# Kernel optimization log

Measured on AMD Instinct MI355X. Metric: run time of the kernel, lower is better.

Reference implementation:

```python
import jax, jax.numpy as jnp
import numpy as np

DIM = 512
HEADS = 8
DIM_HEAD = 64
INNER = HEADS * DIM_HEAD  # 512


def setup_inputs() -> dict:
    key = jax.random.key(0)
    k1, k2, k3 = jax.random.split(key, 3)
    B, N = 4, 2048
    x = jax.random.normal(k1, (B, N, DIM), dtype=jnp.float32)
    # nn.Linear(dim, inner*3, bias=False): weight shape [3*inner, dim]; y = x @ W.T
    w_qkv = jax.random.normal(k2, (3 * INNER, DIM), dtype=jnp.float32) * (DIM ** -0.5)
    # to_out: nn.Linear(inner, dim) with bias
    w_out = jax.random.normal(k3, (DIM, INNER), dtype=jnp.float32) * (INNER ** -0.5)
    b_out = jnp.zeros((DIM,), dtype=jnp.float32)
    return {"x": x, "w_qkv": w_qkv, "w_out": w_out, "b_out": b_out}


def reference(x, w_qkv, w_out, b_out):
    B, N, C = x.shape
    scale = DIM_HEAD ** -0.5
    qkv = jnp.einsum('bnc,fc->bnf', x, w_qkv)  # [B, N, 3*inner]
    qkv = qkv.reshape(B, N, 3, HEADS, DIM_HEAD).transpose(2, 0, 3, 1, 4)  # [3,B,H,N,D]
    q, k, v = qkv[0], qkv[1], qkv[2]
    dots = jnp.einsum('bhnd,bhmd->bhnm', q, k) * scale  # [B,H,N,N]
    attn = jax.nn.softmax(dots, axis=-1)
    out = jnp.einsum('bhnm,bhmd->bhnd', attn, v)  # [B,H,N,D]
    out = out.transpose(0, 2, 1, 3).reshape(B, N, C)
    return jnp.einsum('bnf,cf->bnc', out, w_out) + b_out
```

## Files before the change

kernel.cpp:

```cpp
#include <hip/hip_runtime.h>


typedef __bf16 bf16x8 __attribute__((ext_vector_type(8)));
typedef __bf16 bf16x4v __attribute__((ext_vector_type(4)));
typedef float f32x4 __attribute__((ext_vector_type(4)));
typedef unsigned int u32;
typedef unsigned short u16;
typedef u32 u32x2v __attribute__((ext_vector_type(2)));
typedef u32 u32x4v __attribute__((ext_vector_type(4)));

__device__ __forceinline__ u16 f2bf(float f) {
  union { float f; u32 u; } v; v.f = f;
  u32 r = v.u + 0x7FFFu + ((v.u >> 16) & 1u);
  return (u16)(r >> 16);
}

__device__ __forceinline__ u32x2v pack4bf(float a, float b, float c, float d) {
  bf16x4v v; v[0] = (__bf16)a; v[1] = (__bf16)b; v[2] = (__bf16)c; v[3] = (__bf16)d;
  return __builtin_bit_cast(u32x2v, v);
}

__device__ __forceinline__ f32x4 mfma16(bf16x8 a, bf16x8 b, f32x4 c) {
  return __builtin_amdgcn_mfma_f32_16x16x32_bf16(a, b, c, 0, 0, 0);
}

__device__ __forceinline__ void swap32(u32& a, u32& b) {
  u32x2v r = __builtin_amdgcn_permlane32_swap(a, b, false, false);
  a = r[0]; b = r[1];
}
__device__ __forceinline__ void swap16(u32& a, u32& b) {
  u32x2v r = __builtin_amdgcn_permlane16_swap(a, b, false, false);
  a = r[0]; b = r[1];
}

__global__ void convert_all(const float4* __restrict__ x, const float4* __restrict__ wq,
                            const float4* __restrict__ wo, u16* __restrict__ xb,
                            u16* __restrict__ wqb, u16* __restrict__ wob) {
  int t = blockIdx.x * blockDim.x + threadIdx.x;
  float4 v; u16* dst;
  if (t < 1048576)        { v = x[t];             dst = xb  + (size_t)t * 4; }
  else if (t < 1245184)   { int u = t - 1048576; v = wq[u]; dst = wqb + (size_t)u * 4; }
  else                    { int u = t - 1245184; v = wo[u]; dst = wob + (size_t)u * 4; }
  u32x2v o2;
  o2[0] = (u32)f2bf(v.x) | ((u32)f2bf(v.y) << 16);
  o2[1] = (u32)f2bf(v.z) | ((u32)f2bf(v.w) << 16);
  *(u32x2v*)dst = o2;
}

template<int MODE>
__global__ __launch_bounds__(256, 2) void gemm_nt(
    const u16* __restrict__ A, const u16* __restrict__ B,
    float* __restrict__ Cf, u16* __restrict__ Cb, u16* __restrict__ Vt,
    const float* __restrict__ bias, int M, int N, int K)
{
  __shared__ __align__(16) u16 As[128 * 64];
  __shared__ __align__(16) u16 Bs[128 * 64];
  const int tid = threadIdx.x;
  const int w = tid >> 6, lane = tid & 63, g = lane >> 4, c = lane & 15;
  const int wr = w >> 1, wc = w & 1;
  const int byy = blockIdx.y;
  const int by = (byy & 7) * 8 + (byy >> 3);
  const long m0 = (long)by * 128;
  const long n0 = (long)blockIdx.x * 128;
  const f32x4 zero4 = {0.f, 0.f, 0.f, 0.f};

  f32x4 acc[4][4];
#pragma unroll
  for (int i = 0; i < 4; ++i)
#pragma unroll
    for (int j = 0; j < 4; ++j) acc[i][j] = zero4;

  const int srow = tid >> 3;
  const int sch  = (tid & 7) * 8;

#pragma unroll 1
  for (int kk = 0; kk < K; kk += 64) {
#pragma unroll
    for (int i = 0; i < 4; ++i) {
      __builtin_amdgcn_global_load_lds(
          (__attribute__((address_space(1))) void*)(A + (m0 + i * 32 + srow) * K + kk + sch),
          (__attribute__((address_space(3))) void*)(As + (i * 32 + w * 8) * 64),
          16, 0, 0);
      __builtin_amdgcn_global_load_lds(
          (__attribute__((address_space(1))) void*)(B + (n0 + i * 32 + srow) * K + kk + sch),
          (__attribute__((address_space(3))) void*)(Bs + (i * 32 + w * 8) * 64),
          16, 0, 0);
    }
    __syncthreads();

#pragma unroll
    for (int ks = 0; ks < 2; ++ks) {
      bf16x8 af[4], bfr[4];
#pragma unroll
      for (int mi = 0; mi < 4; ++mi)
        af[mi] = *(const bf16x8*)&As[(wr * 64 + mi * 16 + c) * 64 + ks * 32 + g * 8];
#pragma unroll
      for (int nj = 0; nj < 4; ++nj)
        bfr[nj] = *(const bf16x8*)&Bs[(wc * 64 + nj * 16 + c) * 64 + ks * 32 + g * 8];
#pragma unroll
      for (int mi = 0; mi < 4; ++mi)
#pragma unroll
        for (int nj = 0; nj < 4; ++nj)
          acc[mi][nj] = mfma16(af[mi], bfr[nj], acc[mi][nj]);
    }
    __syncthreads();
  }

#pragma unroll
  for (int mi = 0; mi < 4; ++mi)
#pragma unroll
    for (int nj = 0; nj < 4; ++nj) {
      const long rowb = m0 + wr * 64 + mi * 16 + g * 4;
      const long col  = n0 + wc * 64 + nj * 16 + c;
      if (MODE == 1) {
#pragma unroll
        for (int r = 0; r < 4; ++r)
          Cf[(rowb + r) * N + col] = acc[mi][nj][r] + bias[col];
      } else if (n0 < 512) {
#pragma unroll
        for (int r = 0; r < 4; ++r)
          Cb[(rowb + r) * N + col] = f2bf(acc[mi][nj][r] * 0.18033688f);
      } else if (n0 < 1024) {
#pragma unroll
        for (int r = 0; r < 4; ++r)
          Cb[(rowb + r) * N + col] = f2bf(acc[mi][nj][r]);
      } else {
        u32x2v pk;
        pk[0] = (u32)f2bf(acc[mi][nj][0]) | ((u32)f2bf(acc[mi][nj][1]) << 16);
        pk[1] = (u32)f2bf(acc[mi][nj][2]) | ((u32)f2bf(acc[mi][nj][3]) << 16);
        *(u32x2v*)&Vt[(col - 1024) * 8192 + rowb] = pk;
      }
    }
}

__global__ __launch_bounds__(256, 2) void attn_fwd(const u16* __restrict__ qkv,
                                                   const u16* __restrict__ Vt,
                                                   u16* __restrict__ ao)
{
  __shared__ __align__(16) u16 SH[32768 / 2];
  char* const shb = (char*)SH;

  const int tid = threadIdx.x;
  const int w = tid >> 6, lane = tid & 63, g = lane >> 4, c = lane & 15;

  const int swz = (blockIdx.x & 7) * 64 + (blockIdx.x >> 3);
  const int bh = swz >> 4;
  const int qb = swz & 15;
  const long rowbase = (long)(bh >> 3) * 2048;
  const int hcol = (bh & 7) * 64;
  const int q0 = qb * 128 + w * 32;
  const f32x4 zero4 = {0.f, 0.f, 0.f, 0.f};

  bf16x8 qf[2][2];
#pragma unroll
  for (int sub = 0; sub < 2; ++sub)
#pragma unroll
    for (int ks = 0; ks < 2; ++ks)
      qf[sub][ks] = *(const bf16x8*)(qkv + (rowbase + q0 + sub * 16 + c) * 1536 + hcol + ks * 32 + g * 8);

  float lsum[2] = {0.f, 0.f};
  f32x4 o[2][4];
#pragma unroll
  for (int sub = 0; sub < 2; ++sub)
#pragma unroll
    for (int n = 0; n < 4; ++n) o[sub][n] = zero4;

  const u16* kbase = qkv + rowbase * 1536 + 512 + hcol;
  const u16* vtb   = Vt + (long)hcol * 8192 + rowbase;

  const int srow8 = lane >> 3;
  const int schk8 = ((lane & 7) ^ srow8) * 8;
  const int swzc = (c & 7) << 4;

  const int rd0 = c * 128 + ((g * 16) ^ swzc);
  const int rd1 = c * 128 + ((64 + g * 16) ^ swzc);

  const long r0 = w * 16 + srow8;
  const long r1 = w * 16 + 8 + srow8;
  const u16* kp0 = kbase + (64 + r0) * 1536 + schk8;
  const u16* kp1 = kbase + (64 + r1) * 1536 + schk8;
  const u16* vg0 = vtb + r0 * 8192 + 64 + schk8;
  const u16* vg1 = vtb + r1 * 8192 + 64 + schk8;

  __builtin_amdgcn_global_load_lds(
      (__attribute__((address_space(1))) void*)(kbase + r0 * 1536 + schk8),
      (__attribute__((address_space(3))) void*)(shb + (w * 2 + 0) * 1024), 16, 0, 0);
  __builtin_amdgcn_global_load_lds(
      (__attribute__((address_space(1))) void*)(kbase + r1 * 1536 + schk8),
      (__attribute__((address_space(3))) void*)(shb + (w * 2 + 1) * 1024), 16, 0, 0);
  __builtin_amdgcn_global_load_lds(
      (__attribute__((address_space(1))) void*)(vtb + r0 * 8192 + schk8),
      (__attribute__((address_space(3))) void*)(shb + 16384 + (w * 2 + 0) * 1024), 16, 0, 0);
  __builtin_amdgcn_global_load_lds(
      (__attribute__((address_space(1))) void*)(vtb + r1 * 8192 + schk8),
      (__attribute__((address_space(3))) void*)(shb + 16384 + (w * 2 + 1) * 1024), 16, 0, 0);
  __syncthreads();

  bf16x8 vp[4][2];
  bf16x8 pa[2][2];

#pragma unroll 2
  for (int t = 0; t < 32; ++t) {
    const int buf = t & 1;
    const int KB = buf * 8192;
    const int VB = 16384 + buf * 8192;
    const int KN = 8192 - KB;
    const int VN = 16384 + (8192 - (VB - 16384));

    if (t < 31) {
      __builtin_amdgcn_global_load_lds(
          (__attribute__((address_space(1))) void*)kp0,
          (__attribute__((address_space(3))) void*)(shb + KN + (w * 2 + 0) * 1024), 16, 0, 0);
      __builtin_amdgcn_global_load_lds(
          (__attribute__((address_space(1))) void*)kp1,
          (__attribute__((address_space(3))) void*)(shb + KN + (w * 2 + 1) * 1024), 16, 0, 0);
      __builtin_amdgcn_global_load_lds(
          (__attribute__((address_space(1))) void*)vg0,
          (__attribute__((address_space(3))) void*)(shb + VN + (w * 2 + 0) * 1024), 16, 0, 0);
      __builtin_amdgcn_global_load_lds(
          (__attribute__((address_space(1))) void*)vg1,
          (__attribute__((address_space(3))) void*)(shb + VN + (w * 2 + 1) * 1024), 16, 0, 0);
      kp0 += 64 * 1536; kp1 += 64 * 1536;
      vg0 += 64;        vg1 += 64;
    }

    if (t > 0) {
      __builtin_amdgcn_s_setprio(1);
#pragma unroll
      for (int sub = 0; sub < 2; ++sub)
#pragma unroll
        for (int ks = 0; ks < 2; ++ks)
#pragma unroll
          for (int n = 0; n < 4; ++n)
            o[sub][n] = mfma16(vp[n][ks], pa[sub][ks], o[sub][n]);
      __builtin_amdgcn_s_setprio(0);
    }

    bf16x8 bk[4][2];
#pragma unroll
    for (int n = 0; n < 4; ++n) {
      bk[n][0] = *(const bf16x8*)(shb + KB + n * 2048 + rd0);
      bk[n][1] = *(const bf16x8*)(shb + KB + n * 2048 + rd1);
    }

    f32x4 s[2][4];
    __builtin_amdgcn_s_setprio(1);
#pragma unroll
    for (int sub = 0; sub < 2; ++sub)
#pragma unroll
      for (int n = 0; n < 4; ++n) {
        f32x4 a0 = zero4;
        a0 = mfma16(bk[n][0], qf[sub][0], a0);
        a0 = mfma16(bk[n][1], qf[sub][1], a0);
        s[sub][n] = a0;
      }
    __builtin_amdgcn_s_setprio(0);

#pragma unroll
    for (int sub = 0; sub < 2; ++sub) {
      float rs = 0.f;
      u32 L[4], H[4];
#pragma unroll
      for (int n = 0; n < 4; ++n) {
        float p0 = __builtin_amdgcn_exp2f(s[sub][n][0]);
        float p1 = __builtin_amdgcn_exp2f(s[sub][n][1]);
        float p2 = __builtin_amdgcn_exp2f(s[sub][n][2]);
        float p3 = __builtin_amdgcn_exp2f(s[sub][n][3]);
        rs += (p0 + p1) + (p2 + p3);
        u32x2v pk = pack4bf(p0, p1, p2, p3);
        L[n] = pk[0]; H[n] = pk[1];
      }
      lsum[sub] += rs;
      swap32(L[0], L[1]); swap16(L[0], L[1]);
      swap32(H[0], H[1]); swap16(H[0], H[1]);
      swap32(L[2], L[3]); swap16(L[2], L[3]);
      swap32(H[2], H[3]); swap16(H[2], H[3]);
      u32x4v f0 = {L[0], H[0], L[1], H[1]};
      u32x4v f1 = {L[2], H[2], L[3], H[3]};
      pa[sub][0] = __builtin_bit_cast(bf16x8, f0);
      pa[sub][1] = __builtin_bit_cast(bf16x8, f1);
    }

#pragma unroll
    for (int n = 0; n < 4; ++n) {
      vp[n][0] = *(const bf16x8*)(shb + VB + n * 2048 + rd0);
      vp[n][1] = *(const bf16x8*)(shb + VB + n * 2048 + rd1);
    }

    __syncthreads();
  }

  __builtin_amdgcn_s_setprio(1);
#pragma unroll
  for (int sub = 0; sub < 2; ++sub)
#pragma unroll
    for (int ks = 0; ks < 2; ++ks)
#pragma unroll
      for (int n = 0; n < 4; ++n)
        o[sub][n] = mfma16(vp[n][ks], pa[sub][ks], o[sub][n]);
  __builtin_amdgcn_s_setprio(0);

#pragma unroll
  for (int sub = 0; sub < 2; ++sub) {
    float ls = lsum[sub];
    ls += __shfl_xor(ls, 16);
    ls += __shfl_xor(ls, 32);
    const float linv = 1.0f / ls;
    u16* aor = ao + (rowbase + q0 + sub * 16 + c) * 512 + hcol;
#pragma unroll
    for (int n = 0; n < 4; ++n) {
      u32x2v pk = pack4bf(o[sub][n][0] * linv, o[sub][n][1] * linv,
                          o[sub][n][2] * linv, o[sub][n][3] * linv);
      *(u32x2v*)&aor[n * 16 + g * 4] = pk;
    }
  }
}

extern "C" void kernel_launch(void* const* d_in, const int* in_sizes, int n_in,
                              void* d_out, int out_size, void* d_ws, size_t ws_size,
                              hipStream_t stream) {
  (void)in_sizes; (void)n_in; (void)out_size; (void)ws_size;
  const float* x    = (const float*)d_in[0];
  const float* wqkv = (const float*)d_in[1];
  const float* wout = (const float*)d_in[2];
  const float* bout = (const float*)d_in[3];

  char* ws = (char*)d_ws;
  u16* Xb  = (u16*)(ws);
  u16* Wqb = (u16*)(ws + (8ull << 20));
  u16* Wob = (u16*)(ws + (9ull << 20) + (512ull << 10));
  u16* QKV = (u16*)(ws + (10ull << 20));
  u16* Vt  = (u16*)(ws + (34ull << 20));
  u16* AO  = (u16*)(ws);

  convert_all<<<5120, 256, 0, stream>>>((const float4*)x, (const float4*)wqkv,
                                        (const float4*)wout, Xb, Wqb, Wob);
  gemm_nt<0><<<dim3(12, 64), 256, 0, stream>>>(Xb, Wqb, nullptr, QKV, Vt, nullptr, 8192, 1536, 512);
  attn_fwd<<<512, 256, 0, stream>>>(QKV, Vt, AO);
  gemm_nt<1><<<dim3(4, 64), 256, 0, stream>>>(AO, Wob, (float*)d_out, nullptr, nullptr, bout, 8192, 512, 512);
}
```

Measured before the change: 89.83 us.

## Split KV range across two wave groups per block and merge partials in LDS

The attention block grows from 4 to 8 waves. The two groups of four waves each stream half of the key/value sequence into their own double-buffered LDS region, so the loop runs 16 iterations instead of 32. At the end, the second group writes its partial output accumulators and row sums to LDS, and the first group adds them before normalising and storing. Because the softmax does not subtract a running max, the partials can simply be summed. This doubles the waves per CU to hide latency, at the cost of twice the LDS per block, a tighter register budget from the new launch bounds, and an extra reduction step.

```diff
diff --git a/kernel.cpp b/kernel.cpp
--- a/kernel.cpp
+++ b/kernel.cpp
@@ -133,22 +133,26 @@
     }
 }
 
-__global__ __launch_bounds__(256, 2) void attn_fwd(const u16* __restrict__ qkv,
+__global__ __launch_bounds__(512, 4) void attn_fwd(const u16* __restrict__ qkv,
                                                    const u16* __restrict__ Vt,
                                                    u16* __restrict__ ao)
 {
-  __shared__ __align__(16) u16 SH[32768 / 2];
+  __shared__ __align__(16) u16 SH[65536 / 2];
   char* const shb = (char*)SH;
 
   const int tid = threadIdx.x;
   const int w = tid >> 6, lane = tid & 63, g = lane >> 4, c = lane & 15;
+  const int g2 = w >> 2;
+  const int wq = w & 3;
+  const int GB = g2 << 15;
 
   const int swz = (blockIdx.x & 7) * 64 + (blockIdx.x >> 3);
   const int bh = swz >> 4;
   const int qb = swz & 15;
   const long rowbase = (long)(bh >> 3) * 2048;
   const int hcol = (bh & 7) * 64;
-  const int q0 = qb * 128 + w * 32;
+  const int q0 = qb * 128 + wq * 32;
+  const long kvb = (long)g2 * 1024;
   const f32x4 zero4 = {0.f, 0.f, 0.f, 0.f};
 
   bf16x8 qf[2][2];
@@ -172,54 +176,54 @@
   const int schk8 = ((lane & 7) ^ srow8) * 8;
   const int swzc = (c & 7) << 4;
 
-  const int rd0 = c * 128 + ((g * 16) ^ swzc);
-  const int rd1 = c * 128 + ((64 + g * 16) ^ swzc);
-
-  const long r0 = w * 16 + srow8;
-  const long r1 = w * 16 + 8 + srow8;
-  const u16* kp0 = kbase + (64 + r0) * 1536 + schk8;
-  const u16* kp1 = kbase + (64 + r1) * 1536 + schk8;
-  const u16* vg0 = vtb + r0 * 8192 + 64 + schk8;
-  const u16* vg1 = vtb + r1 * 8192 + 64 + schk8;
+  const int rdG0 = GB + c * 128 + ((g * 16) ^ swzc);
+  const int rdG1 = GB + c * 128 + ((64 + g * 16) ^ swzc);
+
+  const long r0 = wq * 16 + srow8;
+  const long r1 = wq * 16 + 8 + srow8;
+  const u16* kp0 = kbase + (kvb + 64 + r0) * 1536 + schk8;
+  const u16* kp1 = kbase + (kvb + 64 + r1) * 1536 + schk8;
+  const u16* vg0 = vtb + r0 * 8192 + kvb + 64 + schk8;
+  const u16* vg1 = vtb + r1 * 8192 + kvb + 64 + schk8;
 
   __builtin_amdgcn_global_load_lds(
-      (__attribute__((address_space(1))) void*)(kbase + r0 * 1536 + schk8),
-      (__attribute__((address_space(3))) void*)(shb + (w * 2 + 0) * 1024), 16, 0, 0);
+      (__attribute__((address_space(1))) void*)(kbase + (kvb + r0) * 1536 + schk8),
+      (__attribute__((address_space(3))) void*)(shb + GB + (wq * 2 + 0) * 1024), 16, 0, 0);
   __builtin_amdgcn_global_load_lds(
-      (__attribute__((address_space(1))) void*)(kbase + r1 * 1536 + schk8),
-      (__attribute__((address_space(3))) void*)(shb + (w * 2 + 1) * 1024), 16, 0, 0);
+      (__attribute__((address_space(1))) void*)(kbase + (kvb + r1) * 1536 + schk8),
+      (__attribute__((address_space(3))) void*)(shb + GB + (wq * 2 + 1) * 1024), 16, 0, 0);
   __builtin_amdgcn_global_load_lds(
-      (__attribute__((address_space(1))) void*)(vtb + r0 * 8192 + schk8),
-      (__attribute__((address_space(3))) void*)(shb + 16384 + (w * 2 + 0) * 1024), 16, 0, 0);
+      (__attribute__((address_space(1))) void*)(vtb + r0 * 8192 + kvb + schk8),
+      (__attribute__((address_space(3))) void*)(shb + GB + 16384 + (wq * 2 + 0) * 1024), 16, 0, 0);
   __builtin_amdgcn_global_load_lds(
-      (__attribute__((address_space(1))) void*)(vtb + r1 * 8192 + schk8),
-      (__attribute__((address_space(3))) void*)(shb + 16384 + (w * 2 + 1) * 1024), 16, 0, 0);
+      (__attribute__((address_space(1))) void*)(vtb + r1 * 8192 + kvb + schk8),
+      (__attribute__((address_space(3))) void*)(shb + GB + 16384 + (wq * 2 + 1) * 1024), 16, 0, 0);
   __syncthreads();
 
   bf16x8 vp[4][2];
   bf16x8 pa[2][2];
 
 #pragma unroll 2
-  for (int t = 0; t < 32; ++t) {
+  for (int t = 0; t < 16; ++t) {
     const int buf = t & 1;
     const int KB = buf * 8192;
     const int VB = 16384 + buf * 8192;
     const int KN = 8192 - KB;
     const int VN = 16384 + (8192 - (VB - 16384));
 
-    if (t < 31) {
+    if (t < 15) {
       __builtin_amdgcn_global_load_lds(
           (__attribute__((address_space(1))) void*)kp0,
-          (__attribute__((address_space(3))) void*)(shb + KN + (w * 2 + 0) * 1024), 16, 0, 0);
+          (__attribute__((address_space(3))) void*)(shb + GB + KN + (wq * 2 + 0) * 1024), 16, 0, 0);
       __builtin_amdgcn_global_load_lds(
           (__attribute__((address_space(1))) void*)kp1,
-          (__attribute__((address_space(3))) void*)(shb + KN + (w * 2 + 1) * 1024), 16, 0, 0);
+          (__attribute__((address_space(3))) void*)(shb + GB + KN + (wq * 2 + 1) * 1024), 16, 0, 0);
       __builtin_amdgcn_global_load_lds(
           (__attribute__((address_space(1))) void*)vg0,
-          (__attribute__((address_space(3))) void*)(shb + VN + (w * 2 + 0) * 1024), 16, 0, 0);
+          (__attribute__((address_space(3))) void*)(shb + GB + VN + (wq * 2 + 0) * 1024), 16, 0, 0);
       __builtin_amdgcn_global_load_lds(
           (__attribute__((address_space(1))) void*)vg1,
-          (__attribute__((address_space(3))) void*)(shb + VN + (w * 2 + 1) * 1024), 16, 0, 0);
+          (__attribute__((address_space(3))) void*)(shb + GB + VN + (wq * 2 + 1) * 1024), 16, 0, 0);
       kp0 += 64 * 1536; kp1 += 64 * 1536;
       vg0 += 64;        vg1 += 64;
     }
@@ -239,8 +243,8 @@
     bf16x8 bk[4][2];
 #pragma unroll
     for (int n = 0; n < 4; ++n) {
-      bk[n][0] = *(const bf16x8*)(shb + KB + n * 2048 + rd0);
-      bk[n][1] = *(const bf16x8*)(shb + KB + n * 2048 + rd1);
+      bk[n][0] = *(const bf16x8*)(shb + KB + n * 2048 + rdG0);
+      bk[n][1] = *(const bf16x8*)(shb + KB + n * 2048 + rdG1);
     }
 
     f32x4 s[2][4];
@@ -283,8 +287,8 @@
 
 #pragma unroll
     for (int n = 0; n < 4; ++n) {
-      vp[n][0] = *(const bf16x8*)(shb + VB + n * 2048 + rd0);
-      vp[n][1] = *(const bf16x8*)(shb + VB + n * 2048 + rd1);
+      vp[n][0] = *(const bf16x8*)(shb + VB + n * 2048 + rdG0);
+      vp[n][1] = *(const bf16x8*)(shb + VB + n * 2048 + rdG1);
     }
 
     __syncthreads();
@@ -300,18 +304,40 @@
         o[sub][n] = mfma16(vp[n][ks], pa[sub][ks], o[sub][n]);
   __builtin_amdgcn_s_setprio(0);
 
-#pragma unroll
-  for (int sub = 0; sub < 2; ++sub) {
-    float ls = lsum[sub];
-    ls += __shfl_xor(ls, 16);
-    ls += __shfl_xor(ls, 32);
-    const float linv = 1.0f / ls;
-    u16* aor = ao + (rowbase + q0 + sub * 16 + c) * 512 + hcol;
-#pragma unroll
-    for (int n = 0; n < 4; ++n) {
-      u32x2v pk = pack4bf(o[sub][n][0] * linv, o[sub][n][1] * linv,
-                          o[sub][n][2] * linv, o[sub][n][3] * linv);
-      *(u32x2v*)&aor[n * 16 + g * 4] = pk;
+  const int mxor = (lane & 7) << 4;
+  if (g2 == 1) {
+    char* mb = shb + (wq << 13) + lane * 128;
+#pragma unroll
+    for (int sub = 0; sub < 2; ++sub)
+#pragma unroll
+      for (int n = 0; n < 4; ++n)
+        *(f32x4*)(mb + (((sub * 4 + n) * 16) ^ mxor)) = o[sub][n];
+    *(float2*)(shb + 32768 + (wq << 9) + lane * 8) = make_float2(lsum[0], lsum[1]);
+  }
+  __syncthreads();
+  if (g2 == 0) {
+    const char* mb = shb + (wq << 13) + lane * 128;
+#pragma unroll
+    for (int sub = 0; sub < 2; ++sub)
+#pragma unroll
+      for (int n = 0; n < 4; ++n)
+        o[sub][n] += *(const f32x4*)(mb + (((sub * 4 + n) * 16) ^ mxor));
+    float2 lo = *(const float2*)(shb + 32768 + (wq << 9) + lane * 8);
+    lsum[0] += lo.x; lsum[1] += lo.y;
+
+#pragma unroll
+    for (int sub = 0; sub < 2; ++sub) {
+      float ls = lsum[sub];
+      ls += __shfl_xor(ls, 16);
+      ls += __shfl_xor(ls, 32);
+      const float linv = 1.0f / ls;
+      u16* aor = ao + (rowbase + q0 + sub * 16 + c) * 512 + hcol;
+#pragma unroll
+      for (int n = 0; n < 4; ++n) {
+        u32x2v pk = pack4bf(o[sub][n][0] * linv, o[sub][n][1] * linv,
+                            o[sub][n][2] * linv, o[sub][n][3] * linv);
+        *(u32x2v*)&aor[n * 16 + g * 4] = pk;
+      }
     }
   }
 }
@@ -336,6 +362,6 @@
   convert_all<<<5120, 256, 0, stream>>>((const float4*)x, (const float4*)wqkv,
                                         (const float4*)wout, Xb, Wqb, Wob);
   gemm_nt<0><<<dim3(12, 64), 256, 0, stream>>>(Xb, Wqb, nullptr, QKV, Vt, nullptr, 8192, 1536, 512);
-  attn_fwd<<<512, 256, 0, stream>>>(QKV, Vt, AO);
+  attn_fwd<<<512, 512, 0, stream>>>(QKV, Vt, AO);
   gemm_nt<1><<<dim3(4, 64), 256, 0, stream>>>(AO, Wob, (float*)d_out, nullptr, nullptr, bout, 8192, 512, 512);
 }
```

Result: slower. 122.7 us (+36.6%).
